# Performance work log

Measured on AMD Instinct MI355X. Metric: run time of the kernel, lower is better.

Reference implementation:

```python
import math
import jax, jax.numpy as jnp
import numpy as np

D_MODEL, N_HEADS, D_FF = 2048, 16, 8192
B, T = 4, 1024
D_HEAD = D_MODEL // N_HEADS
LN_EPS = 1e-5


def hadamard(x):
    """Orthonormal Hadamard transform along last dim (power-of-two length)."""
    n = x.shape[-1]
    y = x.reshape(-1, n)
    h = 1
    while h < n:
        y = y.reshape(-1, n // (2 * h), 2, h)
        a, b = y[..., 0, :], y[..., 1, :]
        y = jnp.concatenate([a + b, a - b], axis=-1).reshape(-1, n)
        h *= 2
    return (y / math.sqrt(n)).reshape(x.shape)


def quantize_int8_per_row(W):
    s = jnp.maximum(jnp.max(jnp.abs(W), axis=1, keepdims=True), 1e-8) / 127.0
    Q = jnp.clip(jnp.round(W / s), -127, 127).astype(jnp.int8)
    return Q, s


def make_dtdr_weight(key, out_f, in_f):
    W = jax.random.normal(key, (out_f, in_f), dtype=jnp.float32) * 0.02
    return quantize_int8_per_row(hadamard(W))  # W_tilde = W @ H, then int8


def setup_inputs() -> dict:
    key = jax.random.key(0)
    ks = jax.random.split(key, 8)
    x = jax.random.normal(ks[0], (B, T, D_MODEL), dtype=jnp.float32)
    Qq, sq = make_dtdr_weight(ks[1], D_MODEL, D_MODEL)
    Qk, sk = make_dtdr_weight(ks[2], D_MODEL, D_MODEL)
    Qv, sv = make_dtdr_weight(ks[3], D_MODEL, D_MODEL)
    Qo, so = make_dtdr_weight(ks[4], D_MODEL, D_MODEL)
    Qf1, sf1 = make_dtdr_weight(ks[5], D_FF, D_MODEL)
    Qf2, sf2 = make_dtdr_weight(ks[6], D_MODEL, D_FF)
    return dict(
        x=x,
        ln1_g=jnp.ones((D_MODEL,), jnp.float32), ln1_b=jnp.zeros((D_MODEL,), jnp.float32),
        ln2_g=jnp.ones((D_MODEL,), jnp.float32), ln2_b=jnp.zeros((D_MODEL,), jnp.float32),
        Qq=Qq, sq=sq, Qk=Qk, sk=sk, Qv=Qv, sv=sv, Qo=Qo, so=so,
        Qf1=Qf1, sf1=sf1, bf1=jnp.zeros((D_FF,), jnp.float32),
        Qf2=Qf2, sf2=sf2, bf2=jnp.zeros((D_MODEL,), jnp.float32),
    )


def layernorm(x, g, b):
    mu = jnp.mean(x, axis=-1, keepdims=True)
    var = jnp.mean(jnp.square(x - mu), axis=-1, keepdims=True)
    return (x - mu) / jnp.sqrt(var + LN_EPS) * g + b


def dtdr_linear(x, Q, s, bias=None):
    # y = (H x) @ dequant(Q)^T + b
    xh = hadamard(x.astype(jnp.float32))
    W = Q.astype(jnp.float32) * s  # (out, in)
    y = jnp.einsum('btd,od->bto', xh, W)
    return y if bias is None else y + bias


def reference(x, ln1_g, ln1_b, ln2_g, ln2_b, Qq, sq, Qk, sk, Qv, sv, Qo, so,
              Qf1, sf1, bf1, Qf2, sf2, bf2):
    Bc, Tc, C = x.shape
    h = layernorm(x, ln1_g, ln1_b)
    q = dtdr_linear(h, Qq, sq).reshape(Bc, Tc, N_HEADS, D_HEAD).transpose(0, 2, 1, 3)
    k = dtdr_linear(h, Qk, sk).reshape(Bc, Tc, N_HEADS, D_HEAD).transpose(0, 2, 1, 3)
    v = dtdr_linear(h, Qv, sv).reshape(Bc, Tc, N_HEADS, D_HEAD).transpose(0, 2, 1, 3)
    scores = jnp.einsum('bhqd,bhkd->bhqk', q, k) / math.sqrt(D_HEAD)
    p = jax.nn.softmax(scores, axis=-1)
    out = jnp.einsum('bhqk,bhkd->bhqd', p, v)
    out = out.transpose(0, 2, 1, 3).reshape(Bc, Tc, C)
    x = x + dtdr_linear(out, Qo, so)
    h = layernorm(x, ln2_g, ln2_b)
    ff = dtdr_linear(h, Qf1, sf1, bf1)
    ff = jax.nn.gelu(ff, approximate=False)  # torch F.gelu default = erf gelu
    x = x + dtdr_linear(ff, Qf2, sf2, bf2)
    return x
```

## Files before the change

### kernel.cpp

```cpp
#include <hip/hip_runtime.h>
#include <cstdint>
#include <cstddef>

typedef unsigned short u16;
typedef unsigned int   u32;
typedef __bf16 bf16x8 __attribute__((ext_vector_type(8)));
typedef float  f32x4  __attribute__((ext_vector_type(4)));

__device__ __forceinline__ float bf2f(u16 u) {
  union { u32 i; float f; } v; v.i = ((u32)u) << 16; return v.f;
}
__device__ __forceinline__ u16 f2bf(float f) {
  union { float f; u32 i; } v; v.f = f;
  u32 r = v.i + 0x7fffu + ((v.i >> 16) & 1u);
  return (u16)(r >> 16);
}
__device__ __forceinline__ void unpack8(uint4 raw, float* v) {
  v[0]=bf2f(raw.x&0xffff); v[1]=bf2f(raw.x>>16);
  v[2]=bf2f(raw.y&0xffff); v[3]=bf2f(raw.y>>16);
  v[4]=bf2f(raw.z&0xffff); v[5]=bf2f(raw.z>>16);
  v[6]=bf2f(raw.w&0xffff); v[7]=bf2f(raw.w>>16);
}
__device__ __forceinline__ uint4 pack8(const float* v) {
  uint4 r;
  r.x = (u32)f2bf(v[0]) | ((u32)f2bf(v[1])<<16);
  r.y = (u32)f2bf(v[2]) | ((u32)f2bf(v[3])<<16);
  r.z = (u32)f2bf(v[4]) | ((u32)f2bf(v[5])<<16);
  r.w = (u32)f2bf(v[6]) | ((u32)f2bf(v[7])<<16);
  return r;
}
__device__ __forceinline__ void gload16(const void* g, void* l) {
  __builtin_amdgcn_global_load_lds((const __attribute__((address_space(1))) void*)g,
                                   (__attribute__((address_space(3))) void*)l, 16, 0, 0);
}

template<typename T>
__device__ __forceinline__ void load8(const T* p, float* v);
template<> __device__ __forceinline__ void load8<float>(const float* p, float* v) {
  const float4 a = ((const float4*)p)[0];
  const float4 b = ((const float4*)p)[1];
  v[0]=a.x; v[1]=a.y; v[2]=a.z; v[3]=a.w;
  v[4]=b.x; v[5]=b.y; v[6]=b.z; v[7]=b.w;
}
template<> __device__ __forceinline__ void load8<u16>(const u16* p, float* v) {
  unpack8(*(const uint4*)p, v);
}

__global__ __launch_bounds__(256) void cvt_k(const int* __restrict__ Q, u16* __restrict__ W) {
  const size_t i = ((size_t)blockIdx.x * 256 + threadIdx.x) * 8;
  const int4 a = *(const int4*)(Q + i);
  const int4 b = *(const int4*)(Q + i + 4);
  union { float f; u32 u; } c;
  uint4 r;
  u32 t;
  c.f = (float)a.x; t = c.u >> 16; c.f = (float)a.y; r.x = t | (c.u & 0xffff0000u);
  c.f = (float)a.z; t = c.u >> 16; c.f = (float)a.w; r.y = t | (c.u & 0xffff0000u);
  c.f = (float)b.x; t = c.u >> 16; c.f = (float)b.y; r.z = t | (c.u & 0xffff0000u);
  c.f = (float)b.z; t = c.u >> 16; c.f = (float)b.w; r.w = t | (c.u & 0xffff0000u);
  *(uint4*)(W + i) = r;
}

template<typename T>
__global__ __launch_bounds__(256) void ln_fwht_k(const T* __restrict__ X,
    const float* __restrict__ G, const float* __restrict__ Bt, u16* __restrict__ O) {
  __shared__ float buf[2048];
  __shared__ float red[8];
  const int tid = threadIdx.x;
  const int lane = tid & 63, wave = tid >> 6;
  const size_t base = (size_t)blockIdx.x * 2048;
  float v[8]; load8(X + base + tid*8, v);
  float s = 0.f, s2 = 0.f;
  for (int j = 0; j < 8; ++j) { s += v[j]; s2 += v[j]*v[j]; }
  for (int m = 1; m < 64; m <<= 1) { s += __shfl_xor(s, m, 64); s2 += __shfl_xor(s2, m, 64); }
  if (lane == 0) { red[wave] = s; red[4 + wave] = s2; }
  __syncthreads();
  s  = red[0] + red[1] + red[2] + red[3];
  s2 = red[4] + red[5] + red[6] + red[7];
  const float mu = s * (1.f/2048.f);
  const float rstd = rsqrtf(s2 * (1.f/2048.f) - mu*mu + 1e-5f);
  float g[8], bb[8];
  load8(G + tid*8, g); load8(Bt + tid*8, bb);
  for (int j = 0; j < 8; ++j) buf[tid*8 + j] = (v[j] - mu) * rstd * g[j] + bb[j];
  __syncthreads();
  for (int h = 1; h < 2048; h <<= 1) {
    for (int p = 0; p < 4; ++p) {
      const int idx = p*256 + tid;
      const int i = ((idx & ~(h-1)) << 1) | (idx & (h-1));
      const float a = buf[i], c = buf[i + h];
      buf[i] = a + c; buf[i + h] = a - c;
    }
    __syncthreads();
  }
  float o[8];
  for (int j = 0; j < 8; ++j) o[j] = buf[tid*8 + j] * 0.02209708691207961f;
  *(uint4*)&O[base + tid*8] = pack8(o);
}

template<int N>
__global__ __launch_bounds__(256) void fwht_ip(u16* __restrict__ D) {
  __shared__ float buf[N];
  const int tid = threadIdx.x;
  const size_t base = (size_t)blockIdx.x * N;
  constexpr int V8 = N / (8*256);
  for (int i = 0; i < V8; ++i) {
    uint4 raw = *(const uint4*)&D[base + (i*256 + tid)*8];
    float v[8]; unpack8(raw, v);
    for (int j = 0; j < 8; ++j) buf[(i*256 + tid)*8 + j] = v[j];
  }
  __syncthreads();
  constexpr int PAIRS = N / 2 / 256;
  for (int h = 1; h < N; h <<= 1) {
    for (int p = 0; p < PAIRS; ++p) {
      const int idx = p*256 + tid;
      const int i = ((idx & ~(h-1)) << 1) | (idx & (h-1));
      const float a = buf[i], c = buf[i + h];
      buf[i] = a + c; buf[i + h] = a - c;
    }
    __syncthreads();
  }
  const float sc = rsqrtf((float)N);
  for (int i = 0; i < V8; ++i) {
    float v[8];
    for (int j = 0; j < 8; ++j) v[j] = buf[(i*256 + tid)*8 + j] * sc;
    *(uint4*)&D[base + (i*256 + tid)*8] = pack8(v);
  }
}

__global__ __launch_bounds__(256, 2) void gemm_bt(
    const u16* __restrict__ A, const u16* __restrict__ Bw, const float* __restrict__ S,
    void* __restrict__ C, int ldc, int M, int N, int K,
    const float* __restrict__ bias, const float* __restrict__ resf,
    const u16* __restrict__ resb, int dogelu, int outf32)
{
  __shared__ alignas(16) u16 sA[128*32];
  __shared__ alignas(16) u16 sB[128*32];
  const int tid = threadIdx.x;
  const int lane = tid & 63, wave = tid >> 6;
  const int quad = lane >> 4, l16 = lane & 15;
  const int wm = wave & 1, wn = wave >> 1;
  const long tM = (long)blockIdx.x * 128;
  const long tN = (long)blockIdx.y * 128;
  const int sr = lane >> 2;
  const int scol = (lane & 3) * 8;
  f32x4 acc[4][4] = {};
  for (int k0 = 0; k0 < K; k0 += 32) {
#pragma unroll
    for (int i = 0; i < 2; ++i) {
      const int chunk = i*4 + wave;
      const int r = chunk*16 + sr;
      gload16(A  + (size_t)(tM + r)*K + k0 + scol, &sA[chunk*512]);
      gload16(Bw + (size_t)(tN + r)*K + k0 + scol, &sB[chunk*512]);
    }
    __syncthreads();
    bf16x8 af[4], bq[4];
#pragma unroll
    for (int t = 0; t < 4; ++t) af[t] = *(const bf16x8*)&sA[(wm*64 + t*16 + l16)*32 + quad*8];
#pragma unroll
    for (int t = 0; t < 4; ++t) bq[t] = *(const bf16x8*)&sB[(wn*64 + t*16 + l16)*32 + quad*8];
#pragma unroll
    for (int im = 0; im < 4; ++im)
#pragma unroll
      for (int in = 0; in < 4; ++in)
        acc[im][in] = __builtin_amdgcn_mfma_f32_16x16x32_bf16(af[im], bq[in], acc[im][in], 0, 0, 0);
    __syncthreads();
  }
#pragma unroll
  for (int in = 0; in < 4; ++in) {
    const long col = tN + wn*64 + in*16 + l16;
    const float sc = S[col];
    const float bv = bias ? bias[col] : 0.f;
#pragma unroll
    for (int im = 0; im < 4; ++im) {
      const long row0 = tM + wm*64 + im*16 + quad*4;
#pragma unroll
      for (int r = 0; r < 4; ++r) {
        float v = acc[im][in][r] * sc + bv;
        if (dogelu) v = 0.5f * v * (1.f + erff(v * 0.7071067811865475f));
        const size_t off = (size_t)(row0 + r)*ldc + col;
        if (resf) v += resf[off];
        if (resb) v += bf2f(resb[off]);
        if (outf32) ((float*)C)[off] = v;
        else        ((u16*)C)[off]   = f2bf(v);
      }
    }
  }
}

__global__ __launch_bounds__(256, 2) void attn_k(const u16* __restrict__ QKV, u16* __restrict__ O)
{
  __shared__ alignas(16) u16 sKV[16384];
  __shared__ alignas(16) u16 sP[16384];
  const int tid = threadIdx.x;
  const int lane = tid & 63, wave = tid >> 6;
  const int quad = lane >> 4, l16 = lane & 15;
  const int qt = blockIdx.x;
  const int bh = blockIdx.y;
  const int b = bh >> 4, h = bh & 15;
  const size_t rb = (size_t)b * 1024;
  const u16* Qg = QKV + (rb + (size_t)qt*128)*6144 + h*128;
  const u16* Kg = QKV + rb*6144 + 2048 + h*128;
  const u16* Vg = QKV + rb*6144 + 4096 + h*128;

  for (int c = 0; c < 8; ++c) {
    const int chunk = c*4 + wave;
    const int r = chunk*4 + quad;
    gload16(Qg + (size_t)r*6144 + l16*8, &sP[chunk*512]);
  }
  __syncthreads();
  bf16x8 aq[2][4];
  for (int im = 0; im < 2; ++im)
    for (int kk = 0; kk < 4; ++kk)
      aq[im][kk] = *(const bf16x8*)&sP[(wave*32 + im*16 + l16)*128 + kk*32 + quad*8];

  float mrun[2][4], lrun[2][4];
  f32x4 oacc[2][8] = {};
  for (int im = 0; im < 2; ++im)
    for (int r = 0; r < 4; ++r) { mrun[im][r] = -1e30f; lrun[im][r] = 0.f; }

  for (int kt = 0; kt < 8; ++kt) {
    __syncthreads();
    for (int c = 0; c < 8; ++c) {
      const int chunk = c*4 + wave;
      const int r = chunk*4 + quad;
      gload16(Kg + (size_t)(kt*128 + r)*6144 + l16*8, &sKV[chunk*512]);
    }
    __syncthreads();
    f32x4 sf[2][8] = {};
#pragma unroll
    for (int kk = 0; kk < 4; ++kk)
#pragma unroll
      for (int jn = 0; jn < 8; ++jn) {
        const bf16x8 bk = *(const bf16x8*)&sKV[(jn*16 + l16)*128 + kk*32 + quad*8];
        sf[0][jn] = __builtin_amdgcn_mfma_f32_16x16x32_bf16(aq[0][kk], bk, sf[0][jn], 0, 0, 0);
        sf[1][jn] = __builtin_amdgcn_mfma_f32_16x16x32_bf16(aq[1][kk], bk, sf[1][jn], 0, 0, 0);
      }
    const float scale = 0.08838834764831845f;
#pragma unroll
    for (int im = 0; im < 2; ++im)
#pragma unroll
      for (int r = 0; r < 4; ++r) {
        float mx = -1e30f;
        for (int jn = 0; jn < 8; ++jn) mx = fmaxf(mx, sf[im][jn][r] * scale);
        for (int m = 1; m < 16; m <<= 1) mx = fmaxf(mx, __shfl_xor(mx, m, 64));
        const float mold = mrun[im][r];
        const float mnew = fmaxf(mold, mx);
        const float alpha = __expf(mold - mnew);
        float ls = 0.f;
        for (int jn = 0; jn < 8; ++jn) {
          const float p = __expf(sf[im][jn][r] * scale - mnew);
          ls += p;
          sP[wave*4096 + (im*16 + quad*4 + r)*128 + jn*16 + l16] = f2bf(p);
        }
        for (int m = 1; m < 16; m <<= 1) ls += __shfl_xor(ls, m, 64);
        lrun[im][r] = lrun[im][r]*alpha + ls;
        mrun[im][r] = mnew;
        for (int od = 0; od < 8; ++od) oacc[im][od][r] *= alpha;
      }
    __syncthreads();
    for (int c = 0; c < 8; ++c) {
      const int chunk = c*256 + tid;
      const int kv = chunk >> 4;
      const int db = (chunk & 15) * 8;
      const uint4 raw = *(const uint4*)(Vg + (size_t)(kt*128 + kv)*6144 + db);
      const u32 w0[4] = {raw.x, raw.y, raw.z, raw.w};
      for (int j = 0; j < 4; ++j) {
        sKV[(db + 2*j  )*128 + kv] = (u16)(w0[j] & 0xffff);
        sKV[(db + 2*j+1)*128 + kv] = (u16)(w0[j] >> 16);
      }
    }
    __syncthreads();
#pragma unroll
    for (int kk = 0; kk < 4; ++kk) {
      const bf16x8 ap0 = *(const bf16x8*)&sP[wave*4096 + (     l16)*128 + kk*32 + quad*8];
      const bf16x8 ap1 = *(const bf16x8*)&sP[wave*4096 + (16 + l16)*128 + kk*32 + quad*8];
#pragma unroll
      for (int od = 0; od < 8; ++od) {
        const bf16x8 bv = *(const bf16x8*)&sKV[(od*16 + l16)*128 + kk*32 + quad*8];
        oacc[0][od] = __builtin_amdgcn_mfma_f32_16x16x32_bf16(ap0, bv, oacc[0][od], 0, 0, 0);
        oacc[1][od] = __builtin_amdgcn_mfma_f32_16x16x32_bf16(ap1, bv, oacc[1][od], 0, 0, 0);
      }
    }
  }
  for (int im = 0; im < 2; ++im)
    for (int r = 0; r < 4; ++r) {
      const float inv = 1.f / lrun[im][r];
      const size_t row = rb + (size_t)qt*128 + wave*32 + im*16 + quad*4 + r;
      for (int od = 0; od < 8; ++od)
        O[row*2048 + h*128 + od*16 + l16] = f2bf(oacc[im][od][r] * inv);
    }
}

extern "C" void kernel_launch(void* const* d_in, const int* in_sizes, int n_in,
                              void* d_out, int out_size, void* d_ws, size_t ws_size,
                              hipStream_t stream) {
  const float* x    = (const float*)d_in[0];
  const float* ln1g = (const float*)d_in[1];
  const float* ln1b = (const float*)d_in[2];
  const float* ln2g = (const float*)d_in[3];
  const float* ln2b = (const float*)d_in[4];
  const int* Qq  = (const int*)d_in[5];  const float* sq  = (const float*)d_in[6];
  const int* Qk  = (const int*)d_in[7];  const float* sk  = (const float*)d_in[8];
  const int* Qv  = (const int*)d_in[9];  const float* sv  = (const float*)d_in[10];
  const int* Qo  = (const int*)d_in[11]; const float* so  = (const float*)d_in[12];
  const int* Qf1 = (const int*)d_in[13]; const float* sf1 = (const float*)d_in[14];
  const float* bf1 = (const float*)d_in[15];
  const int* Qf2 = (const int*)d_in[16]; const float* sf2 = (const float*)d_in[17];
  const float* bf2 = (const float*)d_in[18];

  u16* XH  = (u16*)d_ws;
  u16* QKV = XH + 8388608;
  u16* FF  = XH + 8388608;
  u16* W   = XH + 41943040;
  float* Xout = (float*)d_out;
  if (ws_size < (size_t)100663296) return;

  ln_fwht_k<float><<<4096, 256, 0, stream>>>(x, ln1g, ln1b, XH);

  cvt_k<<<2048, 256, 0, stream>>>(Qq, W);
  gemm_bt<<<dim3(32,16), 256, 0, stream>>>(XH, W, sq, QKV + 0,    6144, 4096, 2048, 2048, nullptr, nullptr, nullptr, 0, 0);
  cvt_k<<<2048, 256, 0, stream>>>(Qk, W);
  gemm_bt<<<dim3(32,16), 256, 0, stream>>>(XH, W, sk, QKV + 2048, 6144, 4096, 2048, 2048, nullptr, nullptr, nullptr, 0, 0);
  cvt_k<<<2048, 256, 0, stream>>>(Qv, W);
  gemm_bt<<<dim3(32,16), 256, 0, stream>>>(XH, W, sv, QKV + 4096, 6144, 4096, 2048, 2048, nullptr, nullptr, nullptr, 0, 0);

  attn_k<<<dim3(8, 64), 256, 0, stream>>>(QKV, XH);

  fwht_ip<2048><<<4096, 256, 0, stream>>>(XH);

  cvt_k<<<2048, 256, 0, stream>>>(Qo, W);
  gemm_bt<<<dim3(32,16), 256, 0, stream>>>(XH, W, so, Xout, 2048, 4096, 2048, 2048, nullptr, x, nullptr, 0, 1);

  ln_fwht_k<float><<<4096, 256, 0, stream>>>(Xout, ln2g, ln2b, XH);

  cvt_k<<<4096, 256, 0, stream>>>(Qf1, W);
  gemm_bt<<<dim3(32,32), 256, 0, stream>>>(XH, W, sf1,        FF + 0,    8192, 4096, 4096, 2048, bf1,        nullptr, nullptr, 1, 0);
  cvt_k<<<4096, 256, 0, stream>>>(Qf1 + (size_t)4096*2048, W);
  gemm_bt<<<dim3(32,32), 256, 0, stream>>>(XH, W, sf1 + 4096, FF + 4096, 8192, 4096, 4096, 2048, bf1 + 4096, nullptr, nullptr, 1, 0);

  fwht_ip<8192><<<4096, 256, 0, stream>>>(FF);

  cvt_k<<<4096, 256, 0, stream>>>(Qf2, W);
  gemm_bt<<<dim3(32,8), 256, 0, stream>>>(FF, W, sf2,        Xout,        2048, 4096, 1024, 8192, bf2,        Xout,        nullptr, 0, 1);
  cvt_k<<<4096, 256, 0, stream>>>(Qf2 + (size_t)1024*8192, W);
  gemm_bt<<<dim3(32,8), 256, 0, stream>>>(FF, W, sf2 + 1024, Xout + 1024, 2048, 4096, 1024, 8192, bf2 + 1024, Xout + 1024, nullptr, 0, 1);
}
```

Baseline: 1.351 ms.

## Double-buffer GEMM LDS tiles, swizzle workgroup order, merge FF2 into one GEMM

The GEMM kernel now double-buffers its shared-memory A/B tiles. The next K-slice is issued before computing the current one, and one barrier per iteration is removed. Workgroup IDs are remapped in groups of 8 to change tile placement across the chip and improve L2 reuse. The workspace is repartitioned so the full FF2 weight can be converted into the freed XH region and run as a single GEMM with twice the columns, instead of two half GEMMs with a second conversion pass. This costs double the LDS, which may reduce occupancy.

```diff
diff --git a/kernel.cpp b/kernel.cpp
--- a/kernel.cpp
+++ b/kernel.cpp
@@ -132,38 +132,57 @@
     const float* __restrict__ bias, const float* __restrict__ resf,
     const u16* __restrict__ resb, int dogelu, int outf32)
 {
-  __shared__ alignas(16) u16 sA[128*32];
-  __shared__ alignas(16) u16 sB[128*32];
+  __shared__ alignas(16) u16 sA[2][128*32];
+  __shared__ alignas(16) u16 sB[2][128*32];
   const int tid = threadIdx.x;
   const int lane = tid & 63, wave = tid >> 6;
   const int quad = lane >> 4, l16 = lane & 15;
   const int wm = wave & 1, wn = wave >> 1;
-  const long tM = (long)blockIdx.x * 128;
-  const long tN = (long)blockIdx.y * 128;
+  const int nwg = gridDim.x * gridDim.y;
+  int flat = blockIdx.y * gridDim.x + blockIdx.x;
+  if ((nwg & 7) == 0) flat = (flat & 7) * (nwg >> 3) + (flat >> 3);
+  const long tM = (long)(flat % gridDim.x) * 128;
+  const long tN = (long)(flat / gridDim.x) * 128;
   const int sr = lane >> 2;
   const int scol = (lane & 3) * 8;
+  const u16* a0 = A  + (size_t)(tM + wave*16      + sr)*K + scol;
+  const u16* a1 = A  + (size_t)(tM + (wave+4)*16  + sr)*K + scol;
+  const u16* b0 = Bw + (size_t)(tN + wave*16      + sr)*K + scol;
+  const u16* b1 = Bw + (size_t)(tN + (wave+4)*16  + sr)*K + scol;
+
+  auto stage = [&](int buf, int k0) {
+    gload16(a0 + k0, &sA[buf][ wave   *512]);
+    gload16(a1 + k0, &sA[buf][(wave+4)*512]);
+    gload16(b0 + k0, &sB[buf][ wave   *512]);
+    gload16(b1 + k0, &sB[buf][(wave+4)*512]);
+  };
+
   f32x4 acc[4][4] = {};
-  for (int k0 = 0; k0 < K; k0 += 32) {
-#pragma unroll
-    for (int i = 0; i < 2; ++i) {
-      const int chunk = i*4 + wave;
-      const int r = chunk*16 + sr;
-      gload16(A  + (size_t)(tM + r)*K + k0 + scol, &sA[chunk*512]);
-      gload16(Bw + (size_t)(tN + r)*K + k0 + scol, &sB[chunk*512]);
-    }
-    __syncthreads();
+  auto compute = [&](int buf) {
     bf16x8 af[4], bq[4];
 #pragma unroll
-    for (int t = 0; t < 4; ++t) af[t] = *(const bf16x8*)&sA[(wm*64 + t*16 + l16)*32 + quad*8];
-#pragma unroll
-    for (int t = 0; t < 4; ++t) bq[t] = *(const bf16x8*)&sB[(wn*64 + t*16 + l16)*32 + quad*8];
+    for (int t = 0; t < 4; ++t) af[t] = *(const bf16x8*)&sA[buf][(wm*64 + t*16 + l16)*32 + quad*8];
+#pragma unroll
+    for (int t = 0; t < 4; ++t) bq[t] = *(const bf16x8*)&sB[buf][(wn*64 + t*16 + l16)*32 + quad*8];
 #pragma unroll
     for (int im = 0; im < 4; ++im)
 #pragma unroll
       for (int in = 0; in < 4; ++in)
         acc[im][in] = __builtin_amdgcn_mfma_f32_16x16x32_bf16(af[im], bq[in], acc[im][in], 0, 0, 0);
-    __syncthreads();
-  }
+  };
+
+  const int nk = K >> 5;
+  stage(0, 0);
+  __syncthreads();
+  int cur = 0;
+  for (int t = 0; t < nk - 1; ++t) {
+    stage(cur ^ 1, (t + 1) << 5);
+    compute(cur);
+    __syncthreads();
+    cur ^= 1;
+  }
+  compute(cur);
+
 #pragma unroll
   for (int in = 0; in < 4; ++in) {
     const long col = tN + wn*64 + in*16 + l16;
@@ -308,39 +327,38 @@
   const float* bf2 = (const float*)d_in[18];
 
   u16* XH  = (u16*)d_ws;
-  u16* QKV = XH + 8388608;
-  u16* FF  = XH + 8388608;
-  u16* W   = XH + 41943040;
+  u16* Wsl = XH + 8388608;
+  u16* QKV = XH + 16777216;
+  u16* FF  = XH + 16777216;
+  u16* Wf2 = XH;
   float* Xout = (float*)d_out;
   if (ws_size < (size_t)100663296) return;
 
   ln_fwht_k<float><<<4096, 256, 0, stream>>>(x, ln1g, ln1b, XH);
 
-  cvt_k<<<2048, 256, 0, stream>>>(Qq, W);
-  gemm_bt<<<dim3(32,16), 256, 0, stream>>>(XH, W, sq, QKV + 0,    6144, 4096, 2048, 2048, nullptr, nullptr, nullptr, 0, 0);
-  cvt_k<<<2048, 256, 0, stream>>>(Qk, W);
-  gemm_bt<<<dim3(32,16), 256, 0, stream>>>(XH, W, sk, QKV + 2048, 6144, 4096, 2048, 2048, nullptr, nullptr, nullptr, 0, 0);
-  cvt_k<<<2048, 256, 0, stream>>>(Qv, W);
-  gemm_bt<<<dim3(32,16), 256, 0, stream>>>(XH, W, sv, QKV + 4096, 6144, 4096, 2048, 2048, nullptr, nullptr, nullptr, 0, 0);
+  cvt_k<<<2048, 256, 0, stream>>>(Qq, Wsl);
+  gemm_bt<<<dim3(32,16), 256, 0, stream>>>(XH, Wsl, sq, QKV + 0,    6144, 4096, 2048, 2048, nullptr, nullptr, nullptr, 0, 0);
+  cvt_k<<<2048, 256, 0, stream>>>(Qk, Wsl);
+  gemm_bt<<<dim3(32,16), 256, 0, stream>>>(XH, Wsl, sk, QKV + 2048, 6144, 4096, 2048, 2048, nullptr, nullptr, nullptr, 0, 0);
+  cvt_k<<<2048, 256, 0, stream>>>(Qv, Wsl);
+  gemm_bt<<<dim3(32,16), 256, 0, stream>>>(XH, Wsl, sv, QKV + 4096, 6144, 4096, 2048, 2048, nullptr, nullptr, nullptr, 0, 0);
 
   attn_k<<<dim3(8, 64), 256, 0, stream>>>(QKV, XH);
 
   fwht_ip<2048><<<4096, 256, 0, stream>>>(XH);
 
-  cvt_k<<<2048, 256, 0, stream>>>(Qo, W);
-  gemm_bt<<<dim3(32,16), 256, 0, stream>>>(XH, W, so, Xout, 2048, 4096, 2048, 2048, nullptr, x, nullptr, 0, 1);
+  cvt_k<<<2048, 256, 0, stream>>>(Qo, Wsl);
+  gemm_bt<<<dim3(32,16), 256, 0, stream>>>(XH, Wsl, so, Xout, 2048, 4096, 2048, 2048, nullptr, x, nullptr, 0, 1);
 
   ln_fwht_k<float><<<4096, 256, 0, stream>>>(Xout, ln2g, ln2b, XH);
 
-  cvt_k<<<4096, 256, 0, stream>>>(Qf1, W);
-  gemm_bt<<<dim3(32,32), 256, 0, stream>>>(XH, W, sf1,        FF + 0,    8192, 4096, 4096, 2048, bf1,        nullptr, nullptr, 1, 0);
-  cvt_k<<<4096, 256, 0, stream>>>(Qf1 + (size_t)4096*2048, W);
-  gemm_bt<<<dim3(32,32), 256, 0, stream>>>(XH, W, sf1 + 4096, FF + 4096, 8192, 4096, 4096, 2048, bf1 + 4096, nullptr, nullptr, 1, 0);
+  cvt_k<<<4096, 256, 0, stream>>>(Qf1, Wsl);
+  gemm_bt<<<dim3(32,32), 256, 0, stream>>>(XH, Wsl, sf1,        FF + 0,    8192, 4096, 4096, 2048, bf1,        nullptr, nullptr, 1, 0);
+  cvt_k<<<4096, 256, 0, stream>>>(Qf1 + (size_t)4096*2048, Wsl);
+  gemm_bt<<<dim3(32,32), 256, 0, stream>>>(XH, Wsl, sf1 + 4096, FF + 4096, 8192, 4096, 4096, 2048, bf1 + 4096, nullptr, nullptr, 1, 0);
 
   fwht_ip<8192><<<4096, 256, 0, stream>>>(FF);
 
-  cvt_k<<<4096, 256, 0, stream>>>(Qf2, W);
-  gemm_bt<<<dim3(32,8), 256, 0, stream>>>(FF, W, sf2,        Xout,        2048, 4096, 1024, 8192, bf2,        Xout,        nullptr, 0, 1);
-  cvt_k<<<4096, 256, 0, stream>>>(Qf2 + (size_t)1024*8192, W);
-  gemm_bt<<<dim3(32,8), 256, 0, stream>>>(FF, W, sf2 + 1024, Xout + 1024, 2048, 4096, 1024, 8192, bf2 + 1024, Xout + 1024, nullptr, 0, 1);
-}
+  cvt_k<<<8192, 256, 0, stream>>>(Qf2, Wf2);
+  gemm_bt<<<dim3(32,16), 256, 0, stream>>>(FF, Wf2, sf2, Xout, 2048, 4096, 2048, 8192, bf2, Xout, nullptr, 0, 1);
+}
```

New measurement: 1.226 ms. 9.3% less time.
